# Performance work log

Hardware: AMD Instinct MI355X
Metric: run time of the kernel (lower is better)

Reference implementation:

```python
import jax, jax.numpy as jnp
import numpy as np

B, T, F, H, C = 1048576, 11, 3, 11, 7


def setup_inputs() -> dict:
    key = jax.random.key(0)
    ks = jax.random.split(key, 5)
    x = jax.random.normal(ks[0], (B, T, F), dtype=jnp.float32)
    # GRU params (glorot-ish scale); bias is [2, 3H]: row0=input bias, row1=recurrent bias (reset_after=True)
    kernel = jax.random.normal(ks[1], (F, 3 * H), dtype=jnp.float32) * 0.4
    rec_kernel = jax.random.normal(ks[2], (H, 3 * H), dtype=jnp.float32) * 0.2
    bias = jnp.zeros((2, 3 * H), dtype=jnp.float32)
    dense_w = jax.random.normal(ks[3], (T * H, C), dtype=jnp.float32) * 0.1
    dense_b = jnp.zeros((C,), dtype=jnp.float32)
    return {"x": x, "kernel": kernel, "rec_kernel": rec_kernel, "bias": bias,
            "dense_w": dense_w, "dense_b": dense_b}


def _gru(x, kernel, rec_kernel, bias):
    # Keras GRUCell, reset_after=True, inference (no dropout).
    in_b, rec_b = bias[0], bias[1]
    xm = x @ kernel + in_b  # [B,T,3H] precompute input projections

    def step(h, xt):
        inner = h @ rec_kernel + rec_b  # [B,3H]
        xz, xr, xh = jnp.split(xt, 3, axis=-1)
        rz, rr, rh = jnp.split(inner, 3, axis=-1)
        z = jax.nn.sigmoid(xz + rz)
        r = jax.nn.sigmoid(xr + rr)
        hh = jnp.tanh(xh + r * rh)
        h_new = z * h + (1.0 - z) * hh
        return h_new, h_new

    h0 = jnp.zeros((x.shape[0], rec_kernel.shape[0]), x.dtype)
    _, hs = jax.lax.scan(step, h0, jnp.swapaxes(xm, 0, 1))  # [T,B,H]
    return jnp.swapaxes(hs, 0, 1)  # [B,T,H]


def reference(x, kernel, rec_kernel, bias, dense_w, dense_b):
    hs = _gru(x, kernel, rec_kernel, bias)          # [B,T,H]
    flat = hs.reshape(hs.shape[0], -1)              # [B,T*H]
    logits = flat @ dense_w + dense_b               # [B,C]
    return jax.nn.softmax(logits, axis=-1)
```

## Files before the change

kernel.cpp:

```cpp
#include <hip/hip_runtime.h>

#define TT 11
#define FF 3
#define HH 11
#define CC 7
#define TF 33
#define BLOCK 256
#define L2E 1.44269504088896340736f

typedef _Float16 h4 __attribute__((ext_vector_type(4)));
typedef float f4 __attribute__((ext_vector_type(4)));
typedef unsigned int u2 __attribute__((ext_vector_type(2)));

#define WS_GA 0
#define WS_DA 512
#define WS_TOT 1920

__device__ __forceinline__ float fast_sigmoid(float a) {
    float t = __builtin_amdgcn_exp2f(-L2E * a);
    return __builtin_amdgcn_rcpf(1.0f + t);
}
__device__ __forceinline__ float fast_tanh(float a) {
    float t = __builtin_amdgcn_exp2f(-2.0f * L2E * a);
    return fmaf(2.0f, __builtin_amdgcn_rcpf(1.0f + t), -1.0f);
}

__device__ __forceinline__ float gate_val(int g, int k, int n,
        const float* rk, const float* kk, const float* bias) {
    if (n >= HH) return 0.0f;
    if (g == 0 || g == 1) {
        const int col = (g == 0 ? 0 : HH) + n;
        if (k < HH) return rk[k * TF + col];
        if (k < 14) return kk[(k - 11) * TF + col];
        if (k == 14) return bias[col] + bias[TF + col];
        return 0.0f;
    }
    const int col = 2 * HH + n;
    if (g == 2) {
        if (k < HH) return rk[k * TF + col];
        if (k == 14) return bias[TF + col];
        return 0.0f;
    }
    if (k >= 11 && k < 14) return kk[(k - 11) * TF + col];
    if (k == 14) return bias[col];
    return 0.0f;
}

__global__ void prep_weights(const float* __restrict__ k,
                             const float* __restrict__ rk,
                             const float* __restrict__ bias,
                             const float* __restrict__ dw,
                             const float* __restrict__ db,
                             float* __restrict__ ws) {
    const int tid = threadIdx.x;
    unsigned int* wsu = (unsigned int*)ws;
    {
        const int g = tid >> 6, l = tid & 63;
        const int n = l & 15, kb = 4 * (l >> 4);
        unsigned short h[4];
        #pragma unroll
        for (int i = 0; i < 4; ++i) {
            const float v = gate_val(g, kb + i, n, rk, k, bias);
            h[i] = __builtin_bit_cast(unsigned short, (_Float16)v);
        }
        wsu[WS_GA + (g * 64 + l) * 2]     = h[0] | ((unsigned int)h[1] << 16);
        wsu[WS_GA + (g * 64 + l) * 2 + 1] = h[2] | ((unsigned int)h[3] << 16);
    }
    for (int idx = tid; idx < TT * 64; idx += BLOCK) {
        const int t = idx >> 6, l = idx & 63;
        const int c = l & 15, kb = 4 * (l >> 4);
        unsigned short h[4];
        #pragma unroll
        for (int i = 0; i < 4; ++i) {
            const int kk2 = kb + i;
            float v = 0.0f;
            if (c < CC) {
                if (kk2 < HH) v = dw[(t * HH + kk2) * CC + c];
                else if (kk2 == 14 && t == 0) v = db[c];
            }
            h[i] = __builtin_bit_cast(unsigned short, (_Float16)v);
        }
        wsu[WS_DA + idx * 2]     = h[0] | ((unsigned int)h[1] << 16);
        wsu[WS_DA + idx * 2 + 1] = h[2] | ((unsigned int)h[3] << 16);
    }
}

__global__ __launch_bounds__(BLOCK, 5) void gru_main(
    const float* __restrict__ x,
    const float* __restrict__ ws,
    float* __restrict__ out,
    int Bt)
{
    __shared__ unsigned int sxb[BLOCK * TT * 2];
    __shared__ float sda[TT * 64 * 2];
    const int tid = threadIdx.x;
    const long long base = (long long)blockIdx.x * BLOCK;

    for (int i = tid; i < TT * 128; i += BLOCK) sda[i] = ws[WS_DA + i];

    const int lane = tid & 63, wave = tid >> 6;
    const h4* gfp = (const h4*)ws;
    const h4 Az  = gfp[lane];
    const h4 Ar  = gfp[64 + lane];
    const h4 Arh = gfp[128 + lane];
    const h4 Axh = gfp[192 + lane];

    {
        const long long gbase = base * TF;
        const long long gmax = (long long)Bt * TF;
        unsigned short* s16 = (unsigned short*)sxb;
        #pragma unroll
        for (int i = 0; i < TF; ++i) {
            const int e = tid + i * BLOCK;
            const long long g = gbase + e;
            const float v = (g < gmax) ? x[g] : 0.0f;
            const int b = e / TF, r = e % TF;
            const int t = r / FF, s = r % FF;
            const unsigned short hv = __builtin_bit_cast(unsigned short, (_Float16)v);
            const int dw0 = (b * TT + t) * 2;
            if (s == 0) sxb[dw0 + 1] = ((unsigned int)hv) << 16;
            else        s16[dw0 * 2 + (s - 1)] = hv;
        }
    }
    __syncthreads();

    const int q = lane & 15, p = lane >> 4;

    float hD[4][4];
    f4 dC[4];
    #pragma unroll
    for (int k2 = 0; k2 < 4; ++k2) {
        dC[k2] = (f4){0.f, 0.f, 0.f, 0.f};
        #pragma unroll
        for (int r = 0; r < 4; ++r) hD[k2][r] = 0.0f;
    }

    const int xbase = wave * (64 * TT * 2) + q * (TT * 2) + ((p == 2) ? 1 : 0);
    const f4 zf4 = {0.f, 0.f, 0.f, 0.f};

    #pragma unroll 1
    for (int t = 0; t < TT + 1; ++t) {
        const int tx = (t < TT) ? t : (TT - 1);
        h4 Bv[4];
        #pragma unroll
        for (int k2 = 0; k2 < 4; ++k2) {
            const unsigned int xw = sxb[xbase + tx * 2 + k2 * (16 * TT * 2)];
            const unsigned int pk01 =
                (unsigned int)__builtin_bit_cast(unsigned short, (_Float16)hD[k2][0]) |
                ((unsigned int)__builtin_bit_cast(unsigned short, (_Float16)hD[k2][1]) << 16);
            const unsigned int pk23 =
                (unsigned int)__builtin_bit_cast(unsigned short, (_Float16)hD[k2][2]) |
                ((unsigned int)__builtin_bit_cast(unsigned short, (_Float16)hD[k2][3]) << 16);
            const unsigned int c2 =
                (unsigned int)__builtin_bit_cast(unsigned short, (_Float16)hD[k2][2]) | xw;
            const unsigned int b0 = (p == 3) ? xw : pk01;
            const unsigned int b1 = (p <= 1) ? pk23 : ((p == 2) ? c2 : 0x00003C00u);
            const u2 bb = {b0, b1};
            Bv[k2] = __builtin_bit_cast(h4, bb);
        }
        if (t) {
            const h4 dA = *(const h4*)(sda + (t - 1) * 128 + lane * 2);
            #pragma unroll
            for (int k2 = 0; k2 < 4; ++k2)
                dC[k2] = __builtin_amdgcn_mfma_f32_16x16x16f16(dA, Bv[k2], dC[k2], 0, 0, 0);
        }
        if (t < TT) {
            #pragma unroll
            for (int k2 = 0; k2 < 4; ++k2) {
                f4 vz  = __builtin_amdgcn_mfma_f32_16x16x16f16(Az,  Bv[k2], zf4, 0, 0, 0);
                f4 vr  = __builtin_amdgcn_mfma_f32_16x16x16f16(Ar,  Bv[k2], zf4, 0, 0, 0);
                f4 vrh = __builtin_amdgcn_mfma_f32_16x16x16f16(Arh, Bv[k2], zf4, 0, 0, 0);
                f4 vxh = __builtin_amdgcn_mfma_f32_16x16x16f16(Axh, Bv[k2], zf4, 0, 0, 0);
                #pragma unroll
                for (int r = 0; r < 4; ++r) {
                    const float z  = fast_sigmoid(vz[r]);
                    const float rr = fast_sigmoid(vr[r]);
                    const float hh = fast_tanh(fmaf(rr, vrh[r], vxh[r]));
                    hD[k2][r] = hh + z * (hD[k2][r] - hh);
                }
            }
        }
    }

    __syncthreads();
    float* sf = (float*)sxb;
    #pragma unroll
    for (int k2 = 0; k2 < 4; ++k2) {
        const float d0 = dC[k2][0], d1 = dC[k2][1], d2 = dC[k2][2], d3 = dC[k2][3];
        float mloc = fmaxf(fmaxf(d0, d1), d2);
        if (p == 0) mloc = fmaxf(mloc, d3);
        const float m = fmaxf(mloc, __shfl_xor(mloc, 16, 64));
        const float e0 = __builtin_amdgcn_exp2f((d0 - m) * L2E);
        const float e1 = __builtin_amdgcn_exp2f((d1 - m) * L2E);
        const float e2 = __builtin_amdgcn_exp2f((d2 - m) * L2E);
        const float e3 = (p == 0) ? __builtin_amdgcn_exp2f((d3 - m) * L2E) : 0.0f;
        const float sl = e0 + e1 + e2 + e3;
        const float ssum = sl + __shfl_xor(sl, 16, 64);
        const float inv = __builtin_amdgcn_rcpf(ssum);
        if (p < 2) {
            const int bL = wave * 64 + k2 * 16 + q;
            float* dst = sf + bL * CC + p * 4;
            dst[0] = e0 * inv; dst[1] = e1 * inv; dst[2] = e2 * inv;
            if (p == 0) dst[3] = e3 * inv;
        }
    }
    __syncthreads();
    {
        const long long obase = base * CC;
        const long long omax = (long long)Bt * CC;
        #pragma unroll
        for (int i = 0; i < CC; ++i) {
            const long long g = obase + tid + i * BLOCK;
            if (g < omax) out[g] = sf[tid + i * BLOCK];
        }
    }
}

extern "C" void kernel_launch(void* const* d_in, const int* in_sizes, int n_in,
                              void* d_out, int out_size, void* d_ws, size_t ws_size,
                              hipStream_t stream) {
    const float* x  = (const float*)d_in[0];
    const float* k  = (const float*)d_in[1];
    const float* rk = (const float*)d_in[2];
    const float* bi = (const float*)d_in[3];
    const float* dw = (const float*)d_in[4];
    const float* db = (const float*)d_in[5];
    float* out = (float*)d_out;
    float* ws  = (float*)d_ws;

    const int Bt = in_sizes[0] / TF;
    prep_weights<<<1, BLOCK, 0, stream>>>(k, rk, bi, dw, db, ws);
    const int grid = (Bt + BLOCK - 1) / BLOCK;
    gru_main<<<grid, BLOCK, 0, stream>>>(x, ws, out, Bt);
}
```

Baseline: 351.1 us.

## Fold exp2 scaling into gate weights, merge GRU update divisions, shrink LDS

The -log2(e) and -2·log2(e) factors are pre-multiplied into the packed fp16 gate weights and biases, so the per-element multiplies disappear from the recurrence. The z-gate sigmoid and the tanh candidate are folded into one rational expression that needs a single reciprocal instead of two. The staged x tile is split into a 32-bit array and a 16-bit array, which cuts LDS use and allows launch bounds of 7 blocks per CU instead of 5. The risks are overflow to inf or NaN when exp2 saturates in the combined formula, and extra fp16 rounding error from the pre-scaled weights.

```diff
diff --git a/kernel.cpp b/kernel.cpp
--- a/kernel.cpp
+++ b/kernel.cpp
@@ -15,15 +15,6 @@
 #define WS_GA 0
 #define WS_DA 512
 #define WS_TOT 1920
-
-__device__ __forceinline__ float fast_sigmoid(float a) {
-    float t = __builtin_amdgcn_exp2f(-L2E * a);
-    return __builtin_amdgcn_rcpf(1.0f + t);
-}
-__device__ __forceinline__ float fast_tanh(float a) {
-    float t = __builtin_amdgcn_exp2f(-2.0f * L2E * a);
-    return fmaf(2.0f, __builtin_amdgcn_rcpf(1.0f + t), -1.0f);
-}
 
 __device__ __forceinline__ float gate_val(int g, int k, int n,
         const float* rk, const float* kk, const float* bias) {
@@ -57,10 +48,11 @@
     {
         const int g = tid >> 6, l = tid & 63;
         const int n = l & 15, kb = 4 * (l >> 4);
+        const float scale = (g < 2) ? -L2E : (-2.0f * L2E);
         unsigned short h[4];
         #pragma unroll
         for (int i = 0; i < 4; ++i) {
-            const float v = gate_val(g, kb + i, n, rk, k, bias);
+            const float v = gate_val(g, kb + i, n, rk, k, bias) * scale;
             h[i] = __builtin_bit_cast(unsigned short, (_Float16)v);
         }
         wsu[WS_GA + (g * 64 + l) * 2]     = h[0] | ((unsigned int)h[1] << 16);
@@ -85,14 +77,20 @@
     }
 }
 
-__global__ __launch_bounds__(BLOCK, 5) void gru_main(
+__device__ __forceinline__ unsigned int pkf16(float a, float b) {
+    return (unsigned int)__builtin_bit_cast(unsigned short, (_Float16)a) |
+           ((unsigned int)__builtin_bit_cast(unsigned short, (_Float16)b) << 16);
+}
+
+__global__ __launch_bounds__(BLOCK, 7) void gru_main(
     const float* __restrict__ x,
     const float* __restrict__ ws,
     float* __restrict__ out,
     int Bt)
 {
-    __shared__ unsigned int sxb[BLOCK * TT * 2];
-    __shared__ float sda[TT * 64 * 2];
+    __shared__ unsigned int   sxA[BLOCK * TT];
+    __shared__ unsigned short sxB[BLOCK * TT];
+    __shared__ float sda[TT * 128];
     const int tid = threadIdx.x;
     const long long base = (long long)blockIdx.x * BLOCK;
 
@@ -108,7 +106,7 @@
     {
         const long long gbase = base * TF;
         const long long gmax = (long long)Bt * TF;
-        unsigned short* s16 = (unsigned short*)sxb;
+        unsigned short* sxA16 = (unsigned short*)sxA;
         #pragma unroll
         for (int i = 0; i < TF; ++i) {
             const int e = tid + i * BLOCK;
@@ -117,9 +115,8 @@
             const int b = e / TF, r = e % TF;
             const int t = r / FF, s = r % FF;
             const unsigned short hv = __builtin_bit_cast(unsigned short, (_Float16)v);
-            const int dw0 = (b * TT + t) * 2;
-            if (s == 0) sxb[dw0 + 1] = ((unsigned int)hv) << 16;
-            else        s16[dw0 * 2 + (s - 1)] = hv;
+            if (s == 0) sxB[b * TT + t] = hv;
+            else        sxA16[(b * TT + t) * 2 + (s - 1)] = hv;
         }
     }
     __syncthreads();
@@ -135,7 +132,7 @@
         for (int r = 0; r < 4; ++r) hD[k2][r] = 0.0f;
     }
 
-    const int xbase = wave * (64 * TT * 2) + q * (TT * 2) + ((p == 2) ? 1 : 0);
+    const int ibq = (wave * 64 + q) * TT;
     const f4 zf4 = {0.f, 0.f, 0.f, 0.f};
 
     #pragma unroll 1
@@ -144,15 +141,13 @@
         h4 Bv[4];
         #pragma unroll
         for (int k2 = 0; k2 < 4; ++k2) {
-            const unsigned int xw = sxb[xbase + tx * 2 + k2 * (16 * TT * 2)];
-            const unsigned int pk01 =
-                (unsigned int)__builtin_bit_cast(unsigned short, (_Float16)hD[k2][0]) |
-                ((unsigned int)__builtin_bit_cast(unsigned short, (_Float16)hD[k2][1]) << 16);
-            const unsigned int pk23 =
-                (unsigned int)__builtin_bit_cast(unsigned short, (_Float16)hD[k2][2]) |
-                ((unsigned int)__builtin_bit_cast(unsigned short, (_Float16)hD[k2][3]) << 16);
-            const unsigned int c2 =
-                (unsigned int)__builtin_bit_cast(unsigned short, (_Float16)hD[k2][2]) | xw;
+            const int xi = ibq + k2 * (16 * TT) + tx;
+            unsigned int xw = 0;
+            if (p == 3)      xw = sxA[xi];
+            else if (p == 2) xw = ((unsigned int)sxB[xi]) << 16;
+            const unsigned int pk01 = pkf16(hD[k2][0], hD[k2][1]);
+            const unsigned int pk23 = pkf16(hD[k2][2], hD[k2][3]);
+            const unsigned int c2 = (pk23 & 0xFFFFu) | xw;
             const unsigned int b0 = (p == 3) ? xw : pk01;
             const unsigned int b1 = (p <= 1) ? pk23 : ((p == 2) ? c2 : 0x00003C00u);
             const u2 bb = {b0, b1};
@@ -168,22 +163,26 @@
             #pragma unroll
             for (int k2 = 0; k2 < 4; ++k2) {
                 f4 vz  = __builtin_amdgcn_mfma_f32_16x16x16f16(Az,  Bv[k2], zf4, 0, 0, 0);
-                f4 vr  = __builtin_amdgcn_mfma_f32_16x16x16f16(Ar,  Bv[k2], zf4, 0, 0, 0);
+                f4 vv  = __builtin_amdgcn_mfma_f32_16x16x16f16(Ar,  Bv[k2], zf4, 0, 0, 0);
                 f4 vrh = __builtin_amdgcn_mfma_f32_16x16x16f16(Arh, Bv[k2], zf4, 0, 0, 0);
                 f4 vxh = __builtin_amdgcn_mfma_f32_16x16x16f16(Axh, Bv[k2], zf4, 0, 0, 0);
                 #pragma unroll
                 for (int r = 0; r < 4; ++r) {
-                    const float z  = fast_sigmoid(vz[r]);
-                    const float rr = fast_sigmoid(vr[r]);
-                    const float hh = fast_tanh(fmaf(rr, vrh[r], vxh[r]));
-                    hD[k2][r] = hh + z * (hD[k2][r] - hh);
+                    const float tz = __builtin_amdgcn_exp2f(vz[r]);
+                    const float tv = __builtin_amdgcn_exp2f(vv[r]);
+                    const float rr = __builtin_amdgcn_rcpf(1.0f + tv);
+                    const float tu = __builtin_amdgcn_exp2f(fmaf(rr, vrh[r], vxh[r]));
+                    const float hp = hD[k2][r];
+                    const float num = fmaf(tu, hp - tz, hp + tz);
+                    const float den = (1.0f + tz) * (1.0f + tu);
+                    hD[k2][r] = num * __builtin_amdgcn_rcpf(den);
                 }
             }
         }
     }
 
     __syncthreads();
-    float* sf = (float*)sxb;
+    float* sf = (float*)sxA;
     #pragma unroll
     for (int k2 = 0; k2 < 4; ++k2) {
         const float d0 = dC[k2][0], d1 = dC[k2][1], d2 = dC[k2][2], d3 = dC[k2][3];
```

Measured after the change: 326.9 us. -6.9%, faster.
